# Kernel tuning notes

Hardware: AMD Instinct MI355X
Metric: run time of the kernel (lower is better)

The kernel has to match this reference:

```python
import jax, jax.numpy as jnp
import numpy as np


def setup_inputs() -> dict:
    key = jax.random.key(0)
    k1, k2, k3, k4 = jax.random.split(key, 4)
    E, A = 1024, 64
    embedded = jax.random.normal(k1, (4, 4096, E), dtype=jnp.float32)
    # nn.Linear(E, A, bias=False) weight has shape [A, E]; y = x @ W.T
    W_K = jax.random.normal(k2, (A, E), dtype=jnp.float32) * (E ** -0.5)
    W_Q = jax.random.normal(k3, (A, E), dtype=jnp.float32) * (E ** -0.5)
    W_V = jax.random.normal(k4, (A, E), dtype=jnp.float32) * (E ** -0.5)
    return {"embedded": embedded, "W_K": W_K, "W_Q": W_Q, "W_V": W_V}


def reference(embedded, W_K, W_Q, W_V):
    A = W_K.shape[0]
    K = jnp.einsum('bse,ae->bsa', embedded, W_K)
    Q = jnp.einsum('bse,ae->bsa', embedded, W_Q)
    V = jnp.einsum('bse,ae->bsa', embedded, W_V)
    scores = jnp.einsum('bqa,bka->bqk', Q, K) / jnp.sqrt(jnp.float32(A))
    S = K.shape[1]
    causal = jnp.tril(jnp.ones((S, S), dtype=bool))  # True = keep
    scores = jnp.where(causal[None, :, :], scores, -jnp.inf)
    attn = jax.nn.softmax(scores, axis=2)
    out = jnp.einsum('bqk,bka->bqa', attn, V)
    return jnp.round(out, decimals=4)
```

## Files before the change

### kernel.cpp

```cpp
#include <hip/hip_runtime.h>
#include <math.h>

#define B_DIM 4
#define S_DIM 4096
#define E_DIM 1024
#define A_DIM 64
#define M_TOT (B_DIM * S_DIM)

typedef __bf16 v8bf __attribute__((ext_vector_type(8)));
typedef __bf16 v4bf __attribute__((ext_vector_type(4)));
typedef float  v4f  __attribute__((ext_vector_type(4)));

__device__ __forceinline__ v4f mfma16(v8bf a, v8bf b, v4f c) {
    return __builtin_amdgcn_mfma_f32_16x16x32_bf16(a, b, c, 0, 0, 0);
}

__device__ __forceinline__ void lds_dma16(const void* g, void* l) {
    __builtin_amdgcn_global_load_lds(
        (const __attribute__((address_space(1))) unsigned int*)g,
        (__attribute__((address_space(3))) unsigned int*)l, 16, 0, 0);
}

__global__ __launch_bounds__(256) void wconv_kernel(
    const float* __restrict__ Wk, const float* __restrict__ Wq,
    const float* __restrict__ Wv, __bf16* __restrict__ Wb)
{
    const int i = blockIdx.x * 256 + threadIdx.x;
    const int w = i >> 14;
    const int off = (i & 16383) * 4;
    const float* s = ((w == 0) ? Wk : (w == 1) ? Wq : Wv) + off;
    float4 v = *(const float4*)s;
    v4bf o;
    o[0] = (__bf16)v.x; o[1] = (__bf16)v.y; o[2] = (__bf16)v.z; o[3] = (__bf16)v.w;
    *(v4bf*)(Wb + (size_t)w * 65536 + off) = o;
}

__global__ __launch_bounds__(256) void qkv_proj_mfma(
    const float* __restrict__ X,
    const __bf16* __restrict__ Wb,
    __bf16* __restrict__ Kb,
    __bf16* __restrict__ Qb,
    __bf16* __restrict__ Vt)
{
    const int r0   = blockIdx.x * 64;
    const int w    = threadIdx.x >> 6;
    const int lane = threadIdx.x & 63;
    const int L    = lane & 15;
    const int quad = lane >> 4;
    const int cbase = w * 48;

    __shared__ __align__(16) char smem[18432 + 49152];
    __bf16* Xs = (__bf16*)smem;
    __bf16* Bs = (__bf16*)(smem + 18432);
    float (*Tv)[65] = (float(*)[65])smem;

    v4f acc[4][3];
#pragma unroll
    for (int mi = 0; mi < 4; ++mi)
#pragma unroll
        for (int nt = 0; nt < 3; ++nt) acc[mi][nt] = (v4f){0.f, 0.f, 0.f, 0.f};

    const int brow_l  = lane >> 3;
    const int bchunk  = lane & 7;
    const int bgchunk = bchunk ^ brow_l;
    auto stageB = [&](int kc, int buf) {
#pragma unroll
        for (int j = 0; j < 6; ++j) {
            const int rowbase = w * 48 + j * 8;
            const __bf16* g = Wb + (size_t)(rowbase + brow_l) * E_DIM
                              + kc * 64 + bgchunk * 8;
            lds_dma16(g, Bs + buf * 12288 + rowbase * 64);
        }
    };

    const int xrow_i = (lane >> 4);
    const int xcol   = (lane & 15) * 4;
    float4 xr[4];
    auto loadX = [&](int kc) {
#pragma unroll
        for (int i = 0; i < 4; ++i) {
            const int row = i * 16 + w * 4 + xrow_i;
            xr[i] = *(const float4*)(X + (size_t)(r0 + row) * E_DIM + kc * 64 + xcol);
        }
    };
    auto flushX = [&](int buf) {
#pragma unroll
        for (int i = 0; i < 4; ++i) {
            const int row = i * 16 + w * 4 + xrow_i;
            v4bf o;
            o[0] = (__bf16)xr[i].x; o[1] = (__bf16)xr[i].y;
            o[2] = (__bf16)xr[i].z; o[3] = (__bf16)xr[i].w;
            *(v4bf*)(Xs + buf * 4608 + row * 72 + xcol) = o;
        }
    };

    stageB(0, 0);
    loadX(0);
    flushX(0);
    __syncthreads();

#pragma unroll 1
    for (int kc = 0; kc < 16; ++kc) {
        const int cur = kc & 1;
        if (kc < 15) {
            stageB(kc + 1, cur ^ 1);
            loadX(kc + 1);
        }
        v8bf afr[4][2];
#pragma unroll
        for (int mi = 0; mi < 4; ++mi)
#pragma unroll
            for (int ka = 0; ka < 2; ++ka)
                afr[mi][ka] = *(const v8bf*)(Xs + cur * 4608 +
                                (mi * 16 + L) * 72 + ka * 32 + quad * 8);
        v8bf bfr[3][2];
#pragma unroll
        for (int nt = 0; nt < 3; ++nt)
#pragma unroll
            for (int ka = 0; ka < 2; ++ka) {
                const int R = cbase + nt * 16 + L;
                const int slot = (ka * 4 + quad) ^ (R & 7);
                bfr[nt][ka] = *(const v8bf*)(Bs + cur * 12288 + R * 64 + slot * 8);
            }
#pragma unroll
        for (int mi = 0; mi < 4; ++mi)
#pragma unroll
            for (int nt = 0; nt < 3; ++nt)
#pragma unroll
                for (int ka = 0; ka < 2; ++ka)
                    acc[mi][nt] = mfma16(afr[mi][ka], bfr[nt][ka], acc[mi][nt]);

        if (kc < 15) flushX(cur ^ 1);
        __syncthreads();
    }

#pragma unroll
    for (int nt = 0; nt < 3; ++nt) {
        const int c0 = cbase + nt * 16;
        if (c0 < 64) {
#pragma unroll
            for (int mi = 0; mi < 4; ++mi)
#pragma unroll
                for (int r = 0; r < 4; ++r)
                    Kb[(size_t)(r0 + mi * 16 + quad * 4 + r) * A_DIM + c0 + L] =
                        (__bf16)acc[mi][nt][r];
        } else if (c0 < 128) {
#pragma unroll
            for (int mi = 0; mi < 4; ++mi)
#pragma unroll
                for (int r = 0; r < 4; ++r)
                    Qb[(size_t)(r0 + mi * 16 + quad * 4 + r) * A_DIM + (c0 - 64) + L] =
                        (__bf16)(acc[mi][nt][r] * 0.125f);
        } else {
#pragma unroll
            for (int mi = 0; mi < 4; ++mi)
#pragma unroll
                for (int r = 0; r < 4; ++r)
                    Tv[mi * 16 + quad * 4 + r][(c0 - 128) + L] = acc[mi][nt][r];
        }
    }
    __syncthreads();

    {
        const int batch = r0 >> 12;
        const int s0    = r0 & 4095;
        const int a     = threadIdx.x >> 2;
        const int part  = threadIdx.x & 3;
        __bf16* vrow = Vt + (size_t)(batch * 64 + a) * S_DIM + s0 + part * 16;
#pragma unroll
        for (int h = 0; h < 2; ++h) {
            v8bf pk;
#pragma unroll
            for (int j = 0; j < 8; ++j)
                pk[j] = (__bf16)Tv[part * 16 + h * 8 + j][a];
            *(v8bf*)(vrow + h * 8) = pk;
        }
    }
}

__global__ __launch_bounds__(256, 2) void attn_mfma(
    const __bf16* __restrict__ Qb,
    const __bf16* __restrict__ Kb,
    const __bf16* __restrict__ Vt,
    float* __restrict__ P_l,
    float* __restrict__ P_o,
    float* __restrict__ out)
{
    const int b = blockIdx.y;
    const int x = blockIdx.x;
    int qt, ks;
    if (x < 16)      { qt = x;                    ks = 0; }
    else if (x < 48) { qt = 16 + ((x - 16) >> 1); ks = (x - 16) & 1; }
    else if (x < 96) { int y = x - 48; qt = 32 + y / 3;  ks = y % 3; }
    else             { int y = x - 96; qt = 48 + (y >> 2); ks = y & 3; }
    const int nch = (qt >> 4) + 1;

    const int w    = threadIdx.x >> 6;
    const int lane = threadIdx.x & 63;
    const int L    = lane & 15;
    const int quad = lane >> 4;

    __shared__ __align__(16) char smem[67840];
    __bf16 (*Pt)[64][72]   = (__bf16(*)[64][72])smem;
    float*  red_l          = (float*)smem;
    float (*red_o)[64][65] = (float(*)[64][65])(smem + 1024);
    float*  invs           = (float*)(smem + 67584);

    v8bf qf[4][2];
#pragma unroll
    for (int ni = 0; ni < 4; ++ni)
#pragma unroll
        for (int ka = 0; ka < 2; ++ka)
            qf[ni][ka] = *(const v8bf*)(Qb +
                (size_t)(b * S_DIM + qt * 64 + ni * 16 + L) * A_DIM + ka * 32 + quad * 8);

    v4f acc_o[4][4];
#pragma unroll
    for (int i = 0; i < 4; ++i)
#pragma unroll
        for (int j = 0; j < 4; ++j) acc_o[i][j] = (v4f){0.f, 0.f, 0.f, 0.f};
    float lrun[4] = {0.f, 0.f, 0.f, 0.f};

    const int kt0   = ks * 16 + w;
    const int ktmax = min(ks * 16 + 15, qt);

    for (int kt = kt0; kt <= ktmax; kt += 4) {
        v8bf kf[4][2];
#pragma unroll
        for (int mi = 0; mi < 4; ++mi)
#pragma unroll
            for (int ka = 0; ka < 2; ++ka)
                kf[mi][ka] = *(const v8bf*)(Kb +
                    (size_t)(b * S_DIM + kt * 64 + mi * 16 + L) * A_DIM + ka * 32 + quad * 8);
        v8bf vf[4][2];
#pragma unroll
        for (int ma = 0; ma < 4; ++ma)
#pragma unroll
            for (int ki = 0; ki < 2; ++ki)
                vf[ma][ki] = *(const v8bf*)(Vt +
                    (size_t)(b * 64 + ma * 16 + L) * S_DIM + kt * 64 + ki * 32 + quad * 8);

        const bool diag = (kt == qt);

#pragma unroll
        for (int ni = 0; ni < 4; ++ni) {
            v4f s[4];
#pragma unroll
            for (int mi = 0; mi < 4; ++mi) s[mi] = (v4f){0.f, 0.f, 0.f, 0.f};
#pragma unroll
            for (int mi = 0; mi < 4; ++mi)
#pragma unroll
                for (int ka = 0; ka < 2; ++ka)
                    s[mi] = mfma16(kf[mi][ka], qf[ni][ka], s[mi]);

            float rs = 0.f;
#pragma unroll
            for (int mi = 0; mi < 4; ++mi) {
                v4bf p4;
#pragma unroll
                for (int r = 0; r < 4; ++r) {
                    const bool masked = diag && (mi * 16 + quad * 4 + r > ni * 16 + L);
                    const float p = masked ? 0.f : __expf(s[mi][r]);
                    rs += p;
                    p4[r] = (__bf16)p;
                }
                *(v4bf*)&Pt[w][ni * 16 + L][mi * 16 + quad * 4] = p4;
            }
            lrun[ni] += rs;
        }

        v8bf pf[4][2];
#pragma unroll
        for (int ni = 0; ni < 4; ++ni)
#pragma unroll
            for (int ki = 0; ki < 2; ++ki)
                pf[ni][ki] = *(const v8bf*)&Pt[w][ni * 16 + L][ki * 32 + quad * 8];
#pragma unroll
        for (int ma = 0; ma < 4; ++ma)
#pragma unroll
            for (int ni = 0; ni < 4; ++ni)
#pragma unroll
                for (int ki = 0; ki < 2; ++ki)
                    acc_o[ma][ni] = mfma16(vf[ma][ki], pf[ni][ki], acc_o[ma][ni]);
    }

#pragma unroll
    for (int ni = 0; ni < 4; ++ni) {
        lrun[ni] += __shfl_xor(lrun[ni], 16, 64);
        lrun[ni] += __shfl_xor(lrun[ni], 32, 64);
    }

    __syncthreads();

    if (quad == 0) {
#pragma unroll
        for (int ni = 0; ni < 4; ++ni)
            red_l[w * 64 + ni * 16 + L] = lrun[ni];
    }
#pragma unroll
    for (int ma = 0; ma < 4; ++ma)
#pragma unroll
        for (int ni = 0; ni < 4; ++ni)
#pragma unroll
            for (int r = 0; r < 4; ++r)
                red_o[w][ma * 16 + quad * 4 + r][ni * 16 + L] = acc_o[ma][ni][r];
    __syncthreads();

    const int pidx = (b * 64 + qt) * 4 + ks;
    if (threadIdx.x < 64) {
        const int q = threadIdx.x;
        const float denom = red_l[0 * 64 + q] + red_l[1 * 64 + q]
                          + red_l[2 * 64 + q] + red_l[3 * 64 + q];
        if (nch == 1) {
            invs[q] = 1.0f / denom;
        } else {
            P_l[(size_t)pidx * 64 + q] = denom;
            invs[q] = 1.0f;
        }
    }
    __syncthreads();

    {
        const int q  = threadIdx.x >> 2;
        const int ac = (threadIdx.x & 3) << 4;
        const float sc = invs[q];
        float* dst = (nch == 1)
            ? out + (size_t)(b * S_DIM + qt * 64 + q) * A_DIM
            : P_o + (size_t)pidx * 4096 + (size_t)q * 64;
#pragma unroll
        for (int i4 = 0; i4 < 4; ++i4) {
            float vv[4];
#pragma unroll
            for (int j = 0; j < 4; ++j) {
                const int a = ac + i4 * 4 + j;
                vv[j] = sc * (red_o[0][a][q] + red_o[1][a][q]
                            + red_o[2][a][q] + red_o[3][a][q]);
            }
            *(float4*)(dst + ac + i4 * 4) = make_float4(vv[0], vv[1], vv[2], vv[3]);
        }
    }
}

__global__ __launch_bounds__(256) void attn_combine(
    const float* __restrict__ P_l, const float* __restrict__ P_o,
    float* __restrict__ out)
{
    const int qt  = 16 + blockIdx.x;
    const int b   = blockIdx.y;
    const int nch = (qt >> 4) + 1;
    const int base = (b * 64 + qt) * 4;

    __shared__ float inv_s[64];
    if (threadIdx.x < 64) {
        const int q = threadIdx.x;
        float denom = 0.f;
        for (int c = 0; c < nch; ++c)
            denom += P_l[(size_t)(base + c) * 64 + q];
        inv_s[q] = 1.0f / denom;
    }
    __syncthreads();

    const int q  = threadIdx.x >> 2;
    const int ac = (threadIdx.x & 3) << 4;
    const float inv = inv_s[q];
    float* orow = out + (size_t)(b * S_DIM + qt * 64 + q) * A_DIM;
#pragma unroll
    for (int i4 = 0; i4 < 4; ++i4) {
        float4 acc = make_float4(0.f, 0.f, 0.f, 0.f);
        for (int c = 0; c < nch; ++c) {
            float4 v = *(const float4*)(P_o + (size_t)(base + c) * 4096 +
                                        (size_t)q * 64 + ac + i4 * 4);
            acc.x += v.x; acc.y += v.y; acc.z += v.z; acc.w += v.w;
        }
        acc.x *= inv; acc.y *= inv; acc.z *= inv; acc.w *= inv;
        *(float4*)(orow + ac + i4 * 4) = acc;
    }
}

extern "C" void kernel_launch(void* const* d_in, const int* in_sizes, int n_in,
                              void* d_out, int out_size, void* d_ws, size_t ws_size,
                              hipStream_t stream)
{
    const float* X  = (const float*)d_in[0];
    const float* Wk = (const float*)d_in[1];
    const float* Wq = (const float*)d_in[2];
    const float* Wv = (const float*)d_in[3];
    float* out = (float*)d_out;

    __bf16* Kb = (__bf16*)d_ws;
    __bf16* Qb = Kb + (size_t)M_TOT * A_DIM;
    __bf16* Vt = Qb + (size_t)M_TOT * A_DIM;
    __bf16* Wb = Vt + (size_t)M_TOT * A_DIM;
    float*  P_l = (float*)(Wb + 3 * 65536);
    float*  P_o = P_l + 65536;

    wconv_kernel<<<192, 256, 0, stream>>>(Wk, Wq, Wv, Wb);

    qkv_proj_mfma<<<256, 256, 0, stream>>>(X, Wb, Kb, Qb, Vt);

    dim3 g2(160, B_DIM), b2(256);
    attn_mfma<<<g2, b2, 0, stream>>>(Qb, Kb, Vt, P_l, P_o, out);

    dim3 g3(48, B_DIM), b3(256);
    attn_combine<<<g3, b3, 0, stream>>>(P_l, P_o, out);
}
```

Before: 153.9 us.

## Fuse split-K attention and combine into one 8-wave block per query tile

Replaces the split-KV attention kernel plus a separate combine kernel with a single kernel. Each block of 512 threads (8 waves) covers one query tile over the whole causal key range and reduces the partial results in LDS, then writes the final output directly. This removes the global partial buffers, the extra launch and their traffic. In exchange the grid drops from 640 to 256 blocks with uneven per-block work, so causal load imbalance may grow and occupancy may fall.

```diff
diff --git a/kernel.cpp b/kernel.cpp
--- a/kernel.cpp
+++ b/kernel.cpp
@@ -178,33 +178,25 @@
     }
 }
 
-__global__ __launch_bounds__(256, 2) void attn_mfma(
+__global__ __launch_bounds__(512, 2) void attn_fused(
     const __bf16* __restrict__ Qb,
     const __bf16* __restrict__ Kb,
     const __bf16* __restrict__ Vt,
-    float* __restrict__ P_l,
-    float* __restrict__ P_o,
     float* __restrict__ out)
 {
-    const int b = blockIdx.y;
-    const int x = blockIdx.x;
-    int qt, ks;
-    if (x < 16)      { qt = x;                    ks = 0; }
-    else if (x < 48) { qt = 16 + ((x - 16) >> 1); ks = (x - 16) & 1; }
-    else if (x < 96) { int y = x - 48; qt = 32 + y / 3;  ks = y % 3; }
-    else             { int y = x - 96; qt = 48 + (y >> 2); ks = y & 3; }
-    const int nch = (qt >> 4) + 1;
+    const int b  = blockIdx.y;
+    const int qt = blockIdx.x;
 
     const int w    = threadIdx.x >> 6;
     const int lane = threadIdx.x & 63;
     const int L    = lane & 15;
     const int quad = lane >> 4;
 
-    __shared__ __align__(16) char smem[67840];
+    __shared__ __align__(16) char smem[73728];
     __bf16 (*Pt)[64][72]   = (__bf16(*)[64][72])smem;
     float*  red_l          = (float*)smem;
-    float (*red_o)[64][65] = (float(*)[64][65])(smem + 1024);
-    float*  invs           = (float*)(smem + 67584);
+    float (*red_o)[64][65] = (float(*)[64][65])(smem + 2048);
+    float*  invs           = (float*)(smem + 2048 + 66560);
 
     v8bf qf[4][2];
 #pragma unroll
@@ -221,10 +213,7 @@
         for (int j = 0; j < 4; ++j) acc_o[i][j] = (v4f){0.f, 0.f, 0.f, 0.f};
     float lrun[4] = {0.f, 0.f, 0.f, 0.f};
 
-    const int kt0   = ks * 16 + w;
-    const int ktmax = min(ks * 16 + 15, qt);
-
-    for (int kt = kt0; kt <= ktmax; kt += 4) {
+    for (int kt = w; kt <= qt; kt += 8) {
         v8bf kf[4][2];
 #pragma unroll
         for (int mi = 0; mi < 4; ++mi)
@@ -297,38 +286,51 @@
         for (int ni = 0; ni < 4; ++ni)
             red_l[w * 64 + ni * 16 + L] = lrun[ni];
     }
-#pragma unroll
-    for (int ma = 0; ma < 4; ++ma)
-#pragma unroll
-        for (int ni = 0; ni < 4; ++ni)
-#pragma unroll
-            for (int r = 0; r < 4; ++r)
-                red_o[w][ma * 16 + quad * 4 + r][ni * 16 + L] = acc_o[ma][ni][r];
-    __syncthreads();
-
-    const int pidx = (b * 64 + qt) * 4 + ks;
-    if (threadIdx.x < 64) {
-        const int q = threadIdx.x;
-        const float denom = red_l[0 * 64 + q] + red_l[1 * 64 + q]
-                          + red_l[2 * 64 + q] + red_l[3 * 64 + q];
-        if (nch == 1) {
-            invs[q] = 1.0f / denom;
-        } else {
-            P_l[(size_t)pidx * 64 + q] = denom;
-            invs[q] = 1.0f;
-        }
+    if (w >= 4) {
+#pragma unroll
+        for (int ma = 0; ma < 4; ++ma)
+#pragma unroll
+            for (int ni = 0; ni < 4; ++ni)
+#pragma unroll
+                for (int r = 0; r < 4; ++r)
+                    red_o[w - 4][ma * 16 + quad * 4 + r][ni * 16 + L] = acc_o[ma][ni][r];
+    }
+    __syncthreads();
+
+    if (w < 4) {
+#pragma unroll
+        for (int ma = 0; ma < 4; ++ma)
+#pragma unroll
+            for (int ni = 0; ni < 4; ++ni)
+#pragma unroll
+                for (int r = 0; r < 4; ++r)
+                    acc_o[ma][ni][r] += red_o[w][ma * 16 + quad * 4 + r][ni * 16 + L];
+    } else if (w == 4) {
+        float d = 0.f;
+#pragma unroll
+        for (int c = 0; c < 8; ++c) d += red_l[c * 64 + lane];
+        invs[lane] = 1.0f / d;
+    }
+    __syncthreads();
+
+    if (w < 4) {
+#pragma unroll
+        for (int ma = 0; ma < 4; ++ma)
+#pragma unroll
+            for (int ni = 0; ni < 4; ++ni)
+#pragma unroll
+                for (int r = 0; r < 4; ++r)
+                    red_o[w][ma * 16 + quad * 4 + r][ni * 16 + L] = acc_o[ma][ni][r];
     }
     __syncthreads();
 
     {
-        const int q  = threadIdx.x >> 2;
-        const int ac = (threadIdx.x & 3) << 4;
+        const int q  = threadIdx.x >> 3;
+        const int ac = (threadIdx.x & 7) << 3;
         const float sc = invs[q];
-        float* dst = (nch == 1)
-            ? out + (size_t)(b * S_DIM + qt * 64 + q) * A_DIM
-            : P_o + (size_t)pidx * 4096 + (size_t)q * 64;
-#pragma unroll
-        for (int i4 = 0; i4 < 4; ++i4) {
+        float* dst = out + (size_t)(b * S_DIM + qt * 64 + q) * A_DIM + ac;
+#pragma unroll
+        for (int i4 = 0; i4 < 2; ++i4) {
             float vv[4];
 #pragma unroll
             for (int j = 0; j < 4; ++j) {
@@ -336,44 +338,8 @@
                 vv[j] = sc * (red_o[0][a][q] + red_o[1][a][q]
                             + red_o[2][a][q] + red_o[3][a][q]);
             }
-            *(float4*)(dst + ac + i4 * 4) = make_float4(vv[0], vv[1], vv[2], vv[3]);
-        }
-    }
-}
-
-__global__ __launch_bounds__(256) void attn_combine(
-    const float* __restrict__ P_l, const float* __restrict__ P_o,
-    float* __restrict__ out)
-{
-    const int qt  = 16 + blockIdx.x;
-    const int b   = blockIdx.y;
-    const int nch = (qt >> 4) + 1;
-    const int base = (b * 64 + qt) * 4;
-
-    __shared__ float inv_s[64];
-    if (threadIdx.x < 64) {
-        const int q = threadIdx.x;
-        float denom = 0.f;
-        for (int c = 0; c < nch; ++c)
-            denom += P_l[(size_t)(base + c) * 64 + q];
-        inv_s[q] = 1.0f / denom;
-    }
-    __syncthreads();
-
-    const int q  = threadIdx.x >> 2;
-    const int ac = (threadIdx.x & 3) << 4;
-    const float inv = inv_s[q];
-    float* orow = out + (size_t)(b * S_DIM + qt * 64 + q) * A_DIM;
-#pragma unroll
-    for (int i4 = 0; i4 < 4; ++i4) {
-        float4 acc = make_float4(0.f, 0.f, 0.f, 0.f);
-        for (int c = 0; c < nch; ++c) {
-            float4 v = *(const float4*)(P_o + (size_t)(base + c) * 4096 +
-                                        (size_t)q * 64 + ac + i4 * 4);
-            acc.x += v.x; acc.y += v.y; acc.z += v.z; acc.w += v.w;
-        }
-        acc.x *= inv; acc.y *= inv; acc.z *= inv; acc.w *= inv;
-        *(float4*)(orow + ac + i4 * 4) = acc;
+            *(float4*)(dst + i4 * 4) = make_float4(vv[0], vv[1], vv[2], vv[3]);
+        }
     }
 }
 
@@ -391,16 +357,11 @@
     __bf16* Qb = Kb + (size_t)M_TOT * A_DIM;
     __bf16* Vt = Qb + (size_t)M_TOT * A_DIM;
     __bf16* Wb = Vt + (size_t)M_TOT * A_DIM;
-    float*  P_l = (float*)(Wb + 3 * 65536);
-    float*  P_o = P_l + 65536;
 
     wconv_kernel<<<192, 256, 0, stream>>>(Wk, Wq, Wv, Wb);
 
     qkv_proj_mfma<<<256, 256, 0, stream>>>(X, Wb, Kb, Qb, Vt);
 
-    dim3 g2(160, B_DIM), b2(256);
-    attn_mfma<<<g2, b2, 0, stream>>>(Qb, Kb, Vt, P_l, P_o, out);
-
-    dim3 g3(48, B_DIM), b3(256);
-    attn_combine<<<g3, b3, 0, stream>>>(P_l, P_o, out);
-}
+    dim3 g2(64, B_DIM), b2(512);
+    attn_fused<<<g2, b2, 0, stream>>>(Qb, Kb, Vt, out);
+}
```

Result: faster. 146.2 us (-5.0%).
